# Kernel tuning notes

Hardware: AMD Instinct MI355X
Metric: run time of the kernel (lower is better)

The kernel has to match this reference:

```python
import jax, jax.numpy as jnp
import numpy as np

N_SU = 8
DATA_DIM = N_SU * N_SU - 1  # 63
BATCH = 1048576


def _gell_mann(n):
    """Generalized Gell-Mann matrices of su(n), Tr(L_a L_b) = 2 delta_ab."""
    mats = []
    for j in range(n):
        for k in range(j + 1, n):
            m = np.zeros((n, n), dtype=np.complex128); m[j, k] = 1.0; m[k, j] = 1.0
            mats.append(m)
            m = np.zeros((n, n), dtype=np.complex128); m[j, k] = -1.0j; m[k, j] = 1.0j
            mats.append(m)
    for l in range(1, n):
        m = np.zeros((n, n), dtype=np.complex128)
        c = np.sqrt(2.0 / (l * (l + 1)))
        for j in range(l):
            m[j, j] = c
        m[l, l] = -l * c
        mats.append(m)
    return np.stack(mats)


def _structure_const(n):
    """f_abc = Tr([L_a,L_b]L_c)/(4i), d_abc = Tr({L_a,L_b}L_c)/4 (both real)."""
    L = _gell_mann(n)                                  # (D, n, n)
    P = np.einsum('aij,bjk->abik', L, L)               # L_a L_b
    comm = P - P.transpose(1, 0, 2, 3)
    anti = P + P.transpose(1, 0, 2, 3)
    f = (np.einsum('abik,cki->abc', comm, L) / 4.0j).real
    d = (np.einsum('abik,cki->abc', anti, L) / 4.0).real
    return f.astype(np.float32), d.astype(np.float32)

F_CONST, D_CONST = _structure_const(N_SU)              # (D, D, D) each, compile-time constants
TRI = np.stack(np.triu_indices(DATA_DIM, 0))           # incl. diagonal
TRI1 = np.stack(np.triu_indices(DATA_DIM, 1))          # strict upper


def setup_inputs() -> dict:
    key = jax.random.key(0)
    k1, k2, k3, k4, k5 = jax.random.split(key, 5)
    D = DATA_DIM
    return {
        'x': jax.random.normal(k1, (BATCH, D), dtype=jnp.float32),
        'r_x': jax.random.uniform(k2, (D * (D + 1) // 2,), dtype=jnp.float32),
        'r_y': jax.random.uniform(k3, (D * (D - 1) // 2,), dtype=jnp.float32),
        'N': jax.random.uniform(k4, (1,), dtype=jnp.float32),
        'omega': jax.random.uniform(k5, (D,), dtype=jnp.float32),
    }


def _forward(x, r_x, r_y, N, omega):
    f = jnp.asarray(F_CONST)
    d = jnp.asarray(D_CONST)
    D = DATA_DIM
    # NOTE: faithful to the torch source, where `v_x = v_y = torch.zeros(...)`
    # aliases ONE tensor: r_y overwrites r_x on the strict upper triangle and
    # v_x is v_y, which makes c_im exactly zero.
    v = jnp.zeros((D, D), dtype=x.dtype)
    v = v.at[TRI[0], TRI[1]].set(r_x)
    v = v.at[TRI1[0], TRI1[1]].set(r_y)
    v_x = v
    v_y = v
    c_re = v_x.T @ v_x + v_y.T @ v_y                   # einsum('ki,kj->ij', v, v) x2
    c_re = c_re / jnp.trace(c_re)
    c_im = v_x.T @ v_y - v_y.T @ v_x                   # exactly zero (aliasing)
    c_re = N * c_re

    # Precompute the small (D,D) superoperator coefficient matrices once, then
    # apply them to the batch with plain matmuls (bn,mn->bm).
    A1 = jnp.einsum('mjk,ij->mik', f, c_re)
    M_re1 = jnp.einsum('mik,nik->mn', A1, f)           # 'mjk,nik,ij->mn'
    A2 = jnp.einsum('mik,ij->mjk', f, c_re)
    M_re2 = jnp.einsum('mjk,njk->mn', A2, f)           # 'mik,njk,ij->mn'
    B1 = jnp.einsum('mjk,ij->mik', f, c_im)
    M_im1 = jnp.einsum('mik,nik->mn', B1, d)
    B2 = jnp.einsum('mik,ij->mjk', f, c_im)
    M_im2 = jnp.einsum('mjk,njk->mn', B2, d)
    M = -2.0 * M_re1 - 2.0 * M_re2 - 2.0 * M_im1 + 2.0 * M_im2

    d_super_x = x @ M.T                                 # (B, D)
    H = 8.0 * jnp.einsum('kij,k->ij', f, omega)
    h_commutator_x = x @ H.T                            # 'kij,k,bj->bi'
    tr_id = -8.0 * jnp.einsum('imj,ij->m', f, c_im)     # (D,), zero here

    S_x = h_commutator_x + d_super_x
    T_x = x + tr_id
    L_x = S_x + T_x
    return x + 0.01 * L_x


def reference(x, r_x, r_y, N, omega):
    return _forward(x, r_x, r_y, N, omega)
```

## Files before the change

kernel.cpp:

```cpp
#include <hip/hip_runtime.h>
#include <hip/hip_bf16.h>

#define DD 63
#define DD2 (DD * DD)
#define NSU 8
#define TROWS 128

typedef __attribute__((ext_vector_type(8))) short short8;
typedef __attribute__((ext_vector_type(4))) float f32x4;

__device__ float  g_F[DD2 * DD];
__device__ float  g_B[DD * DD2];
__device__ float  g_cc[DD2];
__device__ float  g_scale;
__device__ unsigned short g_Gb[64 * 64];

__device__ __forceinline__ unsigned short f2bf(float f) {
    union { float f; unsigned u; } v; v.f = f;
    unsigned r = v.u + 0x7FFFu + ((v.u >> 16) & 1u);
    return (unsigned short)(r >> 16);
}

__device__ __forceinline__ void fill_L(int a, float (*re)[NSU], float (*im)[NSU]) {
    if (a < 56) {
        int p = a >> 1;
        int j = 0, rem = p;
        while (rem >= 7 - j) { rem -= 7 - j; ++j; }
        int k = j + 1 + rem;
        if ((a & 1) == 0) { re[j][k] = 1.f; re[k][j] = 1.f; }
        else             { im[j][k] = -1.f; im[k][j] = 1.f; }
    } else {
        int l = a - 55;
        float c = sqrtf(2.f / (float)(l * (l + 1)));
        for (int j = 0; j < l; ++j) re[j][j] = c;
        re[l][l] = -(float)l * c;
    }
}

__global__ __launch_bounds__(256) void setup_kernel(const float* __restrict__ r_x,
                                                    const float* __restrict__ r_y,
                                                    const float* __restrict__ Np) {
    const int t = threadIdx.x;
    if (blockIdx.x < DD) {
        const int a = blockIdx.x;
        __shared__ float Ar[NSU][NSU], Ai[NSU][NSU];
        __shared__ float Br[4][NSU][NSU], Bi[4][NSU][NSU];
        __shared__ float Cr[4][NSU][NSU], Ci[4][NSU][NSU];
        const int w = t >> 6, lane = t & 63;
        const int r = lane >> 3, c = lane & 7;
        if (t < 64) { Ar[r][c] = 0.f; Ai[r][c] = 0.f; }
        __syncthreads();
        if (t == 0) fill_L(a, Ar, Ai);
        __syncthreads();
        for (int rb = 0; rb < 16; ++rb) {
            const int b = rb * 4 + w;
            const bool act = (b < DD);
            if (act) { Br[w][r][c] = 0.f; Bi[w][r][c] = 0.f; }
            __syncthreads();
            if (act && lane == 0) fill_L(b, Br[w], Bi[w]);
            __syncthreads();
            if (act) {
                float pr = 0.f, pi = 0.f, qr = 0.f, qi = 0.f;
                #pragma unroll
                for (int k = 0; k < NSU; ++k) {
                    pr += Ar[r][k] * Br[w][k][c] - Ai[r][k] * Bi[w][k][c];
                    pi += Ar[r][k] * Bi[w][k][c] + Ai[r][k] * Br[w][k][c];
                    qr += Br[w][r][k] * Ar[k][c] - Bi[w][r][k] * Ai[k][c];
                    qi += Br[w][r][k] * Ai[k][c] + Bi[w][r][k] * Ar[k][c];
                }
                Cr[w][r][c] = pr - qr;
                Ci[w][r][c] = pi - qi;
            }
            __syncthreads();
            if (act && lane < DD) {
                float im;
                if (lane < 56) {
                    int p = lane >> 1;
                    int j = 0, rem = p;
                    while (rem >= 7 - j) { rem -= 7 - j; ++j; }
                    int k = j + 1 + rem;
                    if ((lane & 1) == 0) im = Ci[w][j][k] + Ci[w][k][j];
                    else                 im = Cr[w][j][k] - Cr[w][k][j];
                } else {
                    int l = lane - 55;
                    float cd = sqrtf(2.f / (float)(l * (l + 1)));
                    float s = 0.f;
                    for (int j = 0; j < l; ++j) s += Ci[w][j][j];
                    im = cd * s - (float)l * cd * Ci[w][l][l];
                }
                g_F[(a * DD + b) * DD + lane] = 0.25f * im;
            }
            __syncthreads();
        }
    } else {
        __shared__ float v[DD2];
        __shared__ float ccs[DD2];
        for (int idx = t; idx < DD2; idx += 256) {
            int i = idx / DD, j = idx % DD;
            float val = 0.f;
            if (j > i)       val = r_y[62 * i - (i * (i - 1)) / 2 + (j - i - 1)];
            else if (j == i) val = r_x[63 * i - (i * (i - 1)) / 2];
            v[idx] = val;
        }
        __syncthreads();
        for (int idx = t; idx < DD2; idx += 256) {
            int i = idx / DD, j = idx % DD;
            float s = 0.f;
            for (int k = 0; k < DD; ++k) s = fmaf(v[k * DD + i], v[k * DD + j], s);
            ccs[idx] = s;
            g_cc[idx] = s;
        }
        __syncthreads();
        if (t == 0) {
            float tr = 0.f;
            for (int i = 0; i < DD; ++i) tr += ccs[i * DD + i];
            g_scale = Np[0] / tr;
        }
    }
}

__global__ __launch_bounds__(256) void buildB_kernel() {
    __shared__ float scc[DD2];
    __shared__ float sf[DD2];
    const int t = threadIdx.x;
    const int n = blockIdx.x;
    for (int idx = t; idx < DD2; idx += 256) {
        scc[idx] = g_cc[idx];
        sf[idx]  = g_F[n * DD2 + idx];
    }
    __syncthreads();
    for (int idx = t; idx < DD2; idx += 256) {
        const int j = idx / DD, k = idx % DD;
        float s = 0.f;
        for (int i = 0; i < DD; ++i) s = fmaf(scc[i * DD + j], sf[i * DD + k], s);
        g_B[n * DD2 + idx] = s;
    }
}

__global__ __launch_bounds__(64) void buildKt_kernel(const float* __restrict__ omega) {
    const int m = blockIdx.x >> 6;
    const int n = blockIdx.x & 63;
    const int lane = threadIdx.x;
    if (m >= DD || n >= DD) {
        if (lane == 0) g_Gb[m * 64 + n] = 0;
        return;
    }
    const float* __restrict__ Fm = g_F + m * DD2;
    const float* __restrict__ Bn = g_B + n * DD2;
    float p = 0.f;
    for (int idx = lane; idx < DD2; idx += 64) p = fmaf(Fm[idx], Bn[idx], p);
    float h = (lane < DD) ? g_F[lane * DD2 + m * DD + n] * omega[lane] : 0.f;
    #pragma unroll
    for (int off = 32; off > 0; off >>= 1) {
        p += __shfl_down(p, off);
        h += __shfl_down(h, off);
    }
    if (lane == 0)
        g_Gb[m * 64 + n] = f2bf(0.01f * (-4.f * g_scale * p + 8.f * h)
                                + ((m == n) ? 1.01f : 0.f));
}

__global__ __launch_bounds__(256, 5) void apply_kernel(const float* __restrict__ x,
                                                       float* __restrict__ out) {
    __shared__ __align__(16) float tile[TROWS * 64];
    const int t = threadIdx.x;
    const size_t base = (size_t)blockIdx.x * (TROWS * DD);

    for (int idx = t; idx < TROWS * DD; idx += 256) {
        const int row = idx / DD;
        const int k = idx - row * DD;
        const int ch = ((k >> 2) ^ (row & 15));
        tile[row * 64 + ch * 4 + (k & 3)] = x[base + idx];
    }
    if (t < TROWS) {
        const int row = t;
        tile[row * 64 + ((15 ^ (row & 15)) << 2) + 3] = 0.f;
    }
    __syncthreads();

    const int w = t >> 6, lane = t & 63;
    const int mrow = lane & 15;
    const int q = lane >> 4;

    const short8* __restrict__ gG = (const short8*)g_Gb;
    short8 bfrag[2][4];
    #pragma unroll
    for (int kt = 0; kt < 2; ++kt)
        #pragma unroll
        for (int nt = 0; nt < 4; ++nt)
            bfrag[kt][nt] = gG[(nt * 16 + mrow) * 8 + kt * 4 + q];

    #pragma unroll
    for (int mt = 0; mt < 2; ++mt) {
        const int row = w * 32 + mt * 16 + mrow;
        const float* __restrict__ rp = tile + row * 64;
        const int rx = row & 15;

        float va[2][8];
        #pragma unroll
        for (int kt = 0; kt < 2; ++kt) {
            const int c0 = kt * 8 + q * 2;
            *(float4*)&va[kt][0] = *(const float4*)&rp[((c0 + 0) ^ rx) * 4];
            *(float4*)&va[kt][4] = *(const float4*)&rp[((c0 + 1) ^ rx) * 4];
        }
        short8 af[2];
        #pragma unroll
        for (int kt = 0; kt < 2; ++kt)
            #pragma unroll
            for (int j = 0; j < 8; ++j) {
                __hip_bfloat16 h = __float2bfloat16(va[kt][j]);
                af[kt][j] = *reinterpret_cast<short*>(&h);
            }

        f32x4 acc[4] = {{0.f,0.f,0.f,0.f},{0.f,0.f,0.f,0.f},
                        {0.f,0.f,0.f,0.f},{0.f,0.f,0.f,0.f}};
        #pragma unroll
        for (int nt = 0; nt < 4; ++nt) {
            acc[nt] = __builtin_amdgcn_mfma_f32_16x16x32_bf16(af[0], bfrag[0][nt], acc[nt], 0, 0, 0);
            acc[nt] = __builtin_amdgcn_mfma_f32_16x16x32_bf16(af[1], bfrag[1][nt], acc[nt], 0, 0, 0);
        }

        #pragma unroll
        for (int nt = 0; nt < 4; ++nt) {
            const int ocol = nt * 16 + mrow;
            if (ocol < DD) {
                #pragma unroll
                for (int r = 0; r < 4; ++r) {
                    const int orow = w * 32 + mt * 16 + q * 4 + r;
                    out[base + orow * DD + ocol] = acc[nt][r];
                }
            }
        }
    }
}

extern "C" void kernel_launch(void* const* d_in, const int* in_sizes, int n_in,
                              void* d_out, int out_size, void* d_ws, size_t ws_size,
                              hipStream_t stream) {
    const float* x     = (const float*)d_in[0];
    const float* r_x   = (const float*)d_in[1];
    const float* r_y   = (const float*)d_in[2];
    const float* Np    = (const float*)d_in[3];
    const float* omega = (const float*)d_in[4];
    float* out = (float*)d_out;

    const int rows = in_sizes[0] / DD;
    const int nblocks = rows / TROWS;

    setup_kernel<<<DD + 1, 256, 0, stream>>>(r_x, r_y, Np);
    buildB_kernel<<<DD, 256, 0, stream>>>();
    buildKt_kernel<<<64 * 64, 64, 0, stream>>>(omega);
    apply_kernel<<<nblocks, 256, 0, stream>>>(x, out);
}
```

Before: 206.9 us.

## Load x directly from global in a persistent wave loop, dropping LDS staging

The apply kernel no longer stages a 128-row tile of x in shared memory behind a block barrier. Each wave now loops grid-stride over 16-row tiles and loads its MFMA A-fragments straight from global memory with scalar per-lane loads. The grid is fixed at 2048 blocks of four waves, and the occupancy hint is removed. This drops the LDS round trip and the barrier, but the global reads become strided per lane rather than fully coalesced, and this pattern relies on the cache to merge accesses.

```diff
diff --git a/kernel.cpp b/kernel.cpp
--- a/kernel.cpp
+++ b/kernel.cpp
@@ -4,7 +4,6 @@
 #define DD 63
 #define DD2 (DD * DD)
 #define NSU 8
-#define TROWS 128
 
 typedef __attribute__((ext_vector_type(8))) short short8;
 typedef __attribute__((ext_vector_type(4))) float f32x4;
@@ -160,27 +159,14 @@
                                 + ((m == n) ? 1.01f : 0.f));
 }
 
-__global__ __launch_bounds__(256, 5) void apply_kernel(const float* __restrict__ x,
-                                                       float* __restrict__ out) {
-    __shared__ __align__(16) float tile[TROWS * 64];
+__global__ __launch_bounds__(256) void apply_kernel(const float* __restrict__ x,
+                                                    float* __restrict__ out,
+                                                    int ntiles, int nwaves) {
     const int t = threadIdx.x;
-    const size_t base = (size_t)blockIdx.x * (TROWS * DD);
-
-    for (int idx = t; idx < TROWS * DD; idx += 256) {
-        const int row = idx / DD;
-        const int k = idx - row * DD;
-        const int ch = ((k >> 2) ^ (row & 15));
-        tile[row * 64 + ch * 4 + (k & 3)] = x[base + idx];
-    }
-    if (t < TROWS) {
-        const int row = t;
-        tile[row * 64 + ((15 ^ (row & 15)) << 2) + 3] = 0.f;
-    }
-    __syncthreads();
-
     const int w = t >> 6, lane = t & 63;
     const int mrow = lane & 15;
     const int q = lane >> 4;
+    const int wave_id = blockIdx.x * 4 + w;
 
     const short8* __restrict__ gG = (const short8*)g_Gb;
     short8 bfrag[2][4];
@@ -190,19 +176,19 @@
         for (int nt = 0; nt < 4; ++nt)
             bfrag[kt][nt] = gG[(nt * 16 + mrow) * 8 + kt * 4 + q];
 
-    #pragma unroll
-    for (int mt = 0; mt < 2; ++mt) {
-        const int row = w * 32 + mt * 16 + mrow;
-        const float* __restrict__ rp = tile + row * 64;
-        const int rx = row & 15;
+    for (int tile = wave_id; tile < ntiles; tile += nwaves) {
+        const size_t tbase = (size_t)tile * (16 * DD);
+        const float* __restrict__ rp = x + tbase + mrow * DD;
 
         float va[2][8];
         #pragma unroll
-        for (int kt = 0; kt < 2; ++kt) {
-            const int c0 = kt * 8 + q * 2;
-            *(float4*)&va[kt][0] = *(const float4*)&rp[((c0 + 0) ^ rx) * 4];
-            *(float4*)&va[kt][4] = *(const float4*)&rp[((c0 + 1) ^ rx) * 4];
-        }
+        for (int kt = 0; kt < 2; ++kt)
+            #pragma unroll
+            for (int j = 0; j < 8; ++j) {
+                int k = kt * 32 + q * 8 + j;
+                if (kt == 1 && j == 7) k = (k == 63) ? 62 : k;
+                va[kt][j] = rp[k];
+            }
         short8 af[2];
         #pragma unroll
         for (int kt = 0; kt < 2; ++kt)
@@ -225,10 +211,8 @@
             const int ocol = nt * 16 + mrow;
             if (ocol < DD) {
                 #pragma unroll
-                for (int r = 0; r < 4; ++r) {
-                    const int orow = w * 32 + mt * 16 + q * 4 + r;
-                    out[base + orow * DD + ocol] = acc[nt][r];
-                }
+                for (int r = 0; r < 4; ++r)
+                    out[tbase + (q * 4 + r) * DD + ocol] = acc[nt][r];
             }
         }
     }
@@ -245,10 +229,12 @@
     float* out = (float*)d_out;
 
     const int rows = in_sizes[0] / DD;
-    const int nblocks = rows / TROWS;
+    const int ntiles = rows / 16;
+    const int ablocks = 2048;
+    const int nwaves = ablocks * 4;
 
     setup_kernel<<<DD + 1, 256, 0, stream>>>(r_x, r_y, Np);
     buildB_kernel<<<DD, 256, 0, stream>>>();
     buildKt_kernel<<<64 * 64, 64, 0, stream>>>(omega);
-    apply_kernel<<<nblocks, 256, 0, stream>>>(x, out);
-}
+    apply_kernel<<<ablocks, 256, 0, stream>>>(x, out, ntiles, nwaves);
+}
```

Result: no change. 210.5 us (+1.7%).
